# Performance work log

Hardware: AMD Instinct MI355X
Metric: run time of the kernel (lower is better)

The kernel has to match this reference:

```python
import jax, jax.numpy as jnp
import numpy as np

HIDDEN = 896
NUM_Q_HEADS = 14
NUM_KV_HEADS = 2
HEAD_DIM = 64
ROPE_BASE = 10000.0
B, S = 4, 2048


def rotate_half(x):
    x1, x2 = jnp.split(x, 2, axis=-1)
    return jnp.concatenate((-x2, x1), axis=-1)


def rope_cos_sin(position_ids):
    # position_ids: [B, S] int -> cos/sin [B, 1, S, HEAD_DIM]
    inv_freq = 1.0 / (ROPE_BASE ** (jnp.arange(0, HEAD_DIM, 2, dtype=jnp.float32) / HEAD_DIM))
    freqs = position_ids.astype(jnp.float32)[..., None] * inv_freq  # [B,S,D/2]
    emb = jnp.concatenate((freqs, freqs), axis=-1)  # [B,S,D]
    return jnp.cos(emb)[:, None, :, :], jnp.sin(emb)[:, None, :, :]


def setup_inputs() -> dict:
    key = jax.random.key(0)
    k1, k2, k3, k4, k5 = jax.random.split(key, 5)
    s = 1.0 / np.sqrt(HIDDEN)
    return {
        "hidden_states": jax.random.normal(k1, (B, S, HIDDEN), dtype=jnp.float32),
        "position_ids": jnp.broadcast_to(jnp.arange(S, dtype=jnp.int64), (B, S)),
        "Wq": jax.random.normal(k2, (HIDDEN, NUM_Q_HEADS * HEAD_DIM), dtype=jnp.float32) * s,
        "Wk": jax.random.normal(k3, (HIDDEN, NUM_KV_HEADS * HEAD_DIM), dtype=jnp.float32) * s,
        "Wv": jax.random.normal(k4, (HIDDEN, NUM_KV_HEADS * HEAD_DIM), dtype=jnp.float32) * s,
        "Wo": jax.random.normal(k5, (NUM_Q_HEADS * HEAD_DIM, HIDDEN), dtype=jnp.float32) * s,
    }


def reference(hidden_states, position_ids, Wq, Wk, Wv, Wo):
    b, s, _ = hidden_states.shape
    n_rep = NUM_Q_HEADS // NUM_KV_HEADS

    q = (hidden_states @ Wq).reshape(b, s, NUM_Q_HEADS, HEAD_DIM).transpose(0, 2, 1, 3)   # [B,Hq,S,D]
    k = (hidden_states @ Wk).reshape(b, s, NUM_KV_HEADS, HEAD_DIM).transpose(0, 2, 1, 3)  # [B,Hkv,S,D]
    v = (hidden_states @ Wv).reshape(b, s, NUM_KV_HEADS, HEAD_DIM).transpose(0, 2, 1, 3)

    cos, sin = rope_cos_sin(position_ids)  # [B,1,S,D]
    q = q * cos + rotate_half(q) * sin
    k = k * cos + rotate_half(k) * sin

    # repeat_interleave KV heads to match query heads
    k = jnp.repeat(k, n_rep, axis=1)  # [B,Hq,S,D]
    v = jnp.repeat(v, n_rep, axis=1)

    scale = 1.0 / jnp.sqrt(jnp.float32(HEAD_DIM))
    attn = jnp.einsum('bhqd,bhkd->bhqk', q, k) * scale  # [B,Hq,S,S]
    attn = jax.nn.softmax(attn, axis=-1)
    out = jnp.einsum('bhqk,bhkd->bhqd', attn, v)  # [B,Hq,S,D]
    out = out.transpose(0, 2, 1, 3).reshape(b, s, NUM_Q_HEADS * HEAD_DIM)
    return out @ Wo
```

## Files before the change

kernel.cpp:

```cpp
#include <hip/hip_runtime.h>
#include <hip/hip_bf16.h>
#include <math.h>

typedef unsigned short ushort_t;
typedef __bf16 bf16x8 __attribute__((ext_vector_type(8)));
typedef float f32x4 __attribute__((ext_vector_type(4)));

#define HIDDEN 896
#define NQH 14
#define NKVH 2
#define HD 64
#define SEQ 2048
#define NBATCH 4

__device__ inline ushort_t f2bf(float x) {
  union { float f; unsigned u; } c; c.f = x;
  unsigned r = c.u + 0x7FFFu + ((c.u >> 16) & 1u);
  return (ushort_t)(r >> 16);
}

__device__ inline unsigned pack2bf(float a, float b) {
  union { float f; unsigned u; } ca, cb; ca.f = a; cb.f = b;
  unsigned ua = ca.u + 0x8000u, ub = cb.u + 0x8000u;
  return __builtin_amdgcn_perm(ub, ua, 0x07060302);
}

__device__ inline bf16x8 ldfrag(const ushort_t* p) {
  return *reinterpret_cast<const bf16x8*>(p);
}

__device__ inline void async16(const ushort_t* g, ushort_t* l) {
  __builtin_amdgcn_global_load_lds(
      (const __attribute__((address_space(1))) void*)g,
      (__attribute__((address_space(3))) void*)l, 16, 0, 0);
}


__device__ inline void transpose_sec(const float* __restrict__ in, ushort_t* __restrict__ out,
                                     int K, int N, int bx, int by) {
  __shared__ float tile[32][33];
  int k0 = by * 32, n0 = bx * 32;
  for (int r = threadIdx.y; r < 32; r += 8) {
    int k = k0 + r, n = n0 + threadIdx.x;
    tile[r][threadIdx.x] = (k < K && n < N) ? in[(size_t)k * N + n] : 0.f;
  }
  __syncthreads();
  for (int r = threadIdx.y; r < 32; r += 8) {
    int n = n0 + r, k = k0 + threadIdx.x;
    if (n < N && k < K) out[(size_t)n * K + k] = f2bf(tile[threadIdx.x][r]);
  }
}

__global__ void k_prep(const float* __restrict__ hidden, ushort_t* __restrict__ hb,
                       const float* __restrict__ Wq, const float* __restrict__ Wk,
                       const float* __restrict__ Wv, const float* __restrict__ Wo,
                       ushort_t* __restrict__ wT, ushort_t* __restrict__ woT,
                       float2* __restrict__ ctab) {
  const int blk = blockIdx.x;
  const int tid = threadIdx.y * 32 + threadIdx.x;
  if (blk < 7168) {
    int i = blk * 256 + tid;
    float4 v = reinterpret_cast<const float4*>(hidden)[i];
    ushort4 o;
    o.x = f2bf(v.x); o.y = f2bf(v.y); o.z = f2bf(v.z); o.w = f2bf(v.w);
    reinterpret_cast<ushort4*>(hb)[i] = o;
  } else if (blk < 7424) {
    int idx = (blk - 7168) * 256 + tid;
    int s = idx >> 5, dp = idx & 31;
    float inv = exp2f(-(float)dp * 0.41524101186092596f);
    float ang = (float)s * inv;
    float sn, cn;
    sincosf(ang, &sn, &cn);
    ctab[idx] = make_float2(cn, sn);
  } else if (blk < 8208) {
    int t = blk - 7424;
    transpose_sec(Wq, wT, 896, 896, t % 28, t / 28);
  } else if (blk < 8320) {
    int t = blk - 8208;
    transpose_sec(Wk, wT + (size_t)896 * 896, 896, 128, t % 4, t / 4);
  } else if (blk < 8432) {
    int t = blk - 8320;
    transpose_sec(Wv, wT + (size_t)1024 * 896, 896, 128, t % 4, t / 4);
  } else {
    int t = blk - 8432;
    transpose_sec(Wo, woT, 896, 896, t % 28, t / 28);
  }
}

__global__ __launch_bounds__(256) void k_qkv(
    const ushort_t* __restrict__ hb,
    const ushort_t* __restrict__ wT,
    const int* __restrict__ pos_ids,
    const float2* __restrict__ ctab,
    ushort_t* __restrict__ Qg,
    ushort_t* __restrict__ Kg,
    ushort_t* __restrict__ Vtg) {
  __shared__ ushort_t smem[8192];
  ushort_t* sa = smem;
  ushort_t* sbb = smem + 4096;

  const int f = blockIdx.x;
  const int x = f & 7, s8 = f >> 3;
  const int sect = s8 % 18;
  const int mt = (s8 / 18) * 8 + x;
  const int nt0 = sect * 64;
  const int m0 = mt * 64;
  const int tid = threadIdx.x;
  const int wave = tid >> 6, lane = tid & 63;
  const int l15 = lane & 15, quad = lane >> 4;
  const int sw = l15 & 7;

  f32x4 acc[4];
  const f32x4 z4 = {0.f, 0.f, 0.f, 0.f};
#pragma unroll
  for (int b = 0; b < 4; ++b) acc[b] = z4;

  for (int kt = 0; kt < 14; ++kt) {
    const int k0 = kt * 64;
    __syncthreads();
#pragma unroll
    for (int i = 0; i < 2; ++i) {
      int id = i * 256 + tid;
      int row = id >> 3;
      int cs = (id & 7) ^ (row & 7);
      async16(hb + (size_t)(m0 + row) * HIDDEN + k0 + cs * 8, sa + (i * 256 + wave * 64) * 8);
      async16(wT + (size_t)(nt0 + row) * HIDDEN + k0 + cs * 8, sbb + (i * 256 + wave * 64) * 8);
    }
    __syncthreads();
#pragma unroll
    for (int kc = 0; kc < 2; ++kc) {
      int c = kc * 4 + quad;
      bf16x8 af = ldfrag(sa + ((wave * 16 + l15) * 8 + (c ^ sw)) * 8);
      bf16x8 bf[4];
#pragma unroll
      for (int nb = 0; nb < 4; ++nb)
        bf[nb] = ldfrag(sbb + ((nb * 16 + l15) * 8 + (c ^ sw)) * 8);
#pragma unroll
      for (int nb = 0; nb < 4; ++nb)
        acc[nb] = __builtin_amdgcn_mfma_f32_16x16x32_bf16(af, bf[nb], acc[nb], 0, 0, 0);
    }
  }

  if (sect < 16) {
    const bool isQ = sect < 14;
    const float csc = isQ ? 0.125f * 1.4426950408889634f : 1.0f;
    ushort_t* dst = isQ ? Qg : Kg;
    const int nheads = isQ ? NQH : NKVH;
    const int hh = isQ ? sect : sect - 14;
#pragma unroll
    for (int r = 0; r < 4; ++r) {
      int token = m0 + wave * 16 + quad * 4 + r;
      int b = token >> 11, s = token & 2047;
      int pos = pos_ids[token];
      size_t base = ((size_t)(b * nheads + hh) * SEQ + s) * HD;
#pragma unroll
      for (int nb = 0; nb < 2; ++nb) {
        float2 cs = ctab[pos * 32 + nb * 16 + l15];
        float x0 = acc[nb][r];
        float x1 = acc[nb + 2][r];
        float y0 = (x0 * cs.x - x1 * cs.y) * csc;
        float y1 = (x1 * cs.x + x0 * cs.y) * csc;
        dst[base + nb * 16 + l15]      = f2bf(y0);
        dst[base + nb * 16 + l15 + 32] = f2bf(y1);
      }
    }
  } else {
    const int kvh = sect - 16;
    __syncthreads();
    ushort_t* vt = smem;
    {
      int tl = wave * 16 + quad * 4;
      int chunk = tl >> 3, ofs = tl & 7;
#pragma unroll
      for (int nb = 0; nb < 4; ++nb) {
        int row = nb * 16 + l15;
        int slot = chunk ^ (row & 7);
        ushort_t* p = vt + row * 64 + slot * 8 + ofs;
        *reinterpret_cast<unsigned*>(p)     = pack2bf(acc[nb][0], acc[nb][1]);
        *reinterpret_cast<unsigned*>(p + 2) = pack2bf(acc[nb][2], acc[nb][3]);
      }
    }
    __syncthreads();
    const int bb = m0 >> 11, s0 = m0 & 2047;
#pragma unroll
    for (int i = 0; i < 2; ++i) {
      int id = i * 256 + tid;
      int row = id >> 3, ch = id & 7;
      int slot = ch ^ (row & 7);
      uint4 v = *reinterpret_cast<const uint4*>(vt + row * 64 + slot * 8);
      *reinterpret_cast<uint4*>(Vtg + ((size_t)(bb * NKVH + kvh) * HD + row) * SEQ + s0 + ch * 8) = v;
    }
  }
}

__global__ __launch_bounds__(256) void k_attn(
    const ushort_t* __restrict__ Qg,
    const ushort_t* __restrict__ Kg,
    const ushort_t* __restrict__ Vtg,
    ushort_t* __restrict__ attn) {
  __shared__ ushort_t kbuf[64 * 64];
  __shared__ ushort_t vbuf[64 * 64];
  __shared__ ushort_t pbuf[4][32 * 72];

  const int f = blockIdx.x;
  const int x = f & 7, s8 = f >> 3;
  const int lh = s8 % 7;
  const int qt = s8 / 7;
  const int b = x >> 1, kvh = x & 1;
  const int h = kvh * 7 + lh;
  const int bh = b * NQH + h;
  const int tid = threadIdx.x;
  const int wave = tid >> 6, lane = tid & 63;
  const int l15 = lane & 15, quad = lane >> 4;
  const int q0 = qt * 128;

  bf16x8 qf[2][2];
#pragma unroll
  for (int qs = 0; qs < 2; ++qs) {
    const size_t qb = ((size_t)bh * SEQ + q0 + wave * 32 + qs * 16 + l15) * HD + quad * 8;
    qf[qs][0] = ldfrag(Qg + qb);
    qf[qs][1] = ldfrag(Qg + qb + 32);
  }

  const size_t kbase = (size_t)(b * NKVH + kvh) * SEQ * HD;
  const size_t vbase = (size_t)(b * NKVH + kvh) * HD * SEQ;

  const int srow = tid >> 3;
  const int sc0 = (tid & 7) ^ (srow & 7);
  const int srow2 = (256 + tid) >> 3;
  const int sc2 = (tid & 7) ^ (srow2 & 7);
  const int sbase1 = wave * 64 * 8;
  const int sbase2 = (256 + wave * 64) * 8;

  float l_part[2] = {0.f, 0.f};
  f32x4 o[2][4];
  const f32x4 z4 = {0.f, 0.f, 0.f, 0.f};
#pragma unroll
  for (int qs = 0; qs < 2; ++qs)
#pragma unroll
    for (int nb = 0; nb < 4; ++nb) o[qs][nb] = z4;

  ushort_t* pw = pbuf[wave];

  for (int jt = 0; jt < 32; ++jt) {
    const int s0 = jt * 64;
    __syncthreads();
    async16(Kg + kbase + (size_t)(s0 + srow) * HD + sc0 * 8, kbuf + sbase1);
    async16(Vtg + vbase + (size_t)srow * SEQ + s0 + sc0 * 8, vbuf + sbase1);
    async16(Kg + kbase + (size_t)(s0 + srow2) * HD + sc2 * 8, kbuf + sbase2);
    async16(Vtg + vbase + (size_t)srow2 * SEQ + s0 + sc2 * 8, vbuf + sbase2);
    __syncthreads();

#pragma unroll
    for (int nb = 0; nb < 4; ++nb) {
      int row = nb * 16 + l15;
      int sw = row & 7;
      bf16x8 kf0 = ldfrag(kbuf + (row * 8 + (quad ^ sw)) * 8);
      bf16x8 kf1 = ldfrag(kbuf + (row * 8 + ((4 + quad) ^ sw)) * 8);
#pragma unroll
      for (int qs = 0; qs < 2; ++qs) {
        f32x4 t = z4;
        t = __builtin_amdgcn_mfma_f32_16x16x32_bf16(kf0, qf[qs][0], t, 0, 0, 0);
        t = __builtin_amdgcn_mfma_f32_16x16x32_bf16(kf1, qf[qs][1], t, 0, 0, 0);
        float p0 = __builtin_amdgcn_exp2f(t[0]);
        float p1 = __builtin_amdgcn_exp2f(t[1]);
        float p2 = __builtin_amdgcn_exp2f(t[2]);
        float p3 = __builtin_amdgcn_exp2f(t[3]);
        l_part[qs] += (p0 + p1) + (p2 + p3);
        uint2 d;
        d.x = pack2bf(p0, p1);
        d.y = pack2bf(p2, p3);
        *reinterpret_cast<uint2*>(pw + (qs * 16 + l15) * 72 + nb * 16 + quad * 4) = d;
      }
    }

    bf16x8 pf[2][2];
#pragma unroll
    for (int qs = 0; qs < 2; ++qs) {
      pf[qs][0] = ldfrag(pw + (qs * 16 + l15) * 72 + quad * 8);
      pf[qs][1] = ldfrag(pw + (qs * 16 + l15) * 72 + 32 + quad * 8);
    }
#pragma unroll
    for (int nb = 0; nb < 4; ++nb) {
      int row = nb * 16 + l15;
      int sw = row & 7;
      bf16x8 vf0 = ldfrag(vbuf + (row * 8 + (quad ^ sw)) * 8);
      bf16x8 vf1 = ldfrag(vbuf + (row * 8 + ((4 + quad) ^ sw)) * 8);
#pragma unroll
      for (int qs = 0; qs < 2; ++qs) {
        o[qs][nb] = __builtin_amdgcn_mfma_f32_16x16x32_bf16(pf[qs][0], vf0, o[qs][nb], 0, 0, 0);
        o[qs][nb] = __builtin_amdgcn_mfma_f32_16x16x32_bf16(pf[qs][1], vf1, o[qs][nb], 0, 0, 0);
      }
    }
  }

#pragma unroll
  for (int qs = 0; qs < 2; ++qs) {
    float s = l_part[qs];
    s += __shfl_xor(s, 16);
    s += __shfl_xor(s, 32);
    l_part[qs] = s;
  }

#pragma unroll
  for (int qs = 0; qs < 2; ++qs) {
    float il = 1.0f / l_part[qs];
#pragma unroll
    for (int r = 0; r < 4; ++r) {
      float inv = __shfl(il, quad * 4 + r);
      int qg = q0 + wave * 32 + qs * 16 + quad * 4 + r;
#pragma unroll
      for (int nb = 0; nb < 4; ++nb) {
        float val = o[qs][nb][r] * inv;
        attn[(size_t)(b * SEQ + qg) * (NQH * HD) + h * HD + nb * 16 + l15] = f2bf(val);
      }
    }
  }
}

__global__ __launch_bounds__(256) void k_oproj(
    const ushort_t* __restrict__ attn,
    const ushort_t* __restrict__ woT,
    float* __restrict__ out) {
  __shared__ ushort_t smem[8192];
  ushort_t* sa = smem;
  ushort_t* sbb = smem + 4096;

  const int f = blockIdx.x;
  const int x = f & 7, s8 = f >> 3;
  const int n_sect = s8 % 14;
  const int mt = (s8 / 14) * 8 + x;
  const int n0 = n_sect * 64;
  const int m0 = mt * 64;
  const int tid = threadIdx.x;
  const int wave = tid >> 6, lane = tid & 63;
  const int l15 = lane & 15, quad = lane >> 4;
  const int sw = l15 & 7;

  f32x4 acc[4];
  const f32x4 z4 = {0.f, 0.f, 0.f, 0.f};
#pragma unroll
  for (int b = 0; b < 4; ++b) acc[b] = z4;

  for (int kt = 0; kt < 14; ++kt) {
    const int k0 = kt * 64;
    __syncthreads();
#pragma unroll
    for (int i = 0; i < 2; ++i) {
      int id = i * 256 + tid;
      int row = id >> 3;
      int cs = (id & 7) ^ (row & 7);
      async16(attn + (size_t)(m0 + row) * HIDDEN + k0 + cs * 8, sa + (i * 256 + wave * 64) * 8);
      async16(woT + (size_t)(n0 + row) * HIDDEN + k0 + cs * 8, sbb + (i * 256 + wave * 64) * 8);
    }
    __syncthreads();
#pragma unroll
    for (int kc = 0; kc < 2; ++kc) {
      int c = kc * 4 + quad;
      bf16x8 af = ldfrag(sa + ((wave * 16 + l15) * 8 + (c ^ sw)) * 8);
      bf16x8 bf[4];
#pragma unroll
      for (int nb = 0; nb < 4; ++nb)
        bf[nb] = ldfrag(sbb + ((nb * 16 + l15) * 8 + (c ^ sw)) * 8);
#pragma unroll
      for (int nb = 0; nb < 4; ++nb)
        acc[nb] = __builtin_amdgcn_mfma_f32_16x16x32_bf16(af, bf[nb], acc[nb], 0, 0, 0);
    }
  }

#pragma unroll
  for (int nb = 0; nb < 4; ++nb)
#pragma unroll
    for (int r = 0; r < 4; ++r)
      out[(size_t)(m0 + wave * 16 + quad * 4 + r) * HIDDEN +
          n0 + nb * 16 + l15] = acc[nb][r];
}


extern "C" void kernel_launch(void* const* d_in, const int* in_sizes, int n_in,
                              void* d_out, int out_size, void* d_ws, size_t ws_size,
                              hipStream_t stream) {
  (void)in_sizes; (void)n_in; (void)out_size; (void)ws_size;
  const float* hidden = (const float*)d_in[0];
  const int* pos      = (const int*)d_in[1];
  const float* Wq     = (const float*)d_in[2];
  const float* Wk     = (const float*)d_in[3];
  const float* Wv     = (const float*)d_in[4];
  const float* Wo     = (const float*)d_in[5];
  float* out = (float*)d_out;

  char* ws = (char*)d_ws;
  ushort_t* hb   = (ushort_t*)(ws);
  ushort_t* wT   = (ushort_t*)(ws + 14680064);
  float2*   ctab = (float2*)  (ws + 16744448);
  ushort_t* Qg   = (ushort_t*)(ws + 17268736);
  ushort_t* Kg   = (ushort_t*)(ws + 31948800);
  ushort_t* Vtg  = (ushort_t*)(ws + 34045952);
  ushort_t* attn = (ushort_t*)(ws + 36143104);
  ushort_t* woT  = (ushort_t*)(ws + 50823168);

  k_prep<<<9216, dim3(32, 8), 0, stream>>>(hidden, hb, Wq, Wk, Wv, Wo, wT, woT, ctab);
  k_qkv<<<2304, 256, 0, stream>>>(hb, wT, pos, ctab, Qg, Kg, Vtg);
  k_attn<<<896, 256, 0, stream>>>(Qg, Kg, Vtg, attn);
  k_oproj<<<1792, 256, 0, stream>>>(attn, woT, out);
}
```

Measured before the change: 226.9 us.

## Enlarge QKV and output-projection GEMM tiles to 128x128 with 2x2 wave layout

Both projection GEMMs move from 64x64 block tiles, where each wave computed 16x64, to 128x128 tiles where each wave computes a 64x64 sub-tile of 4x4 MFMA accumulators. This raises arithmetic intensity and cuts redundant global and LDS traffic per FLOP. The QKV epilogue is reworked so each wave handles one head for RoPE, and the V transpose goes through a per-wave LDS region. In exchange, the grids shrink to 576 and 448 blocks, which may underfill the GPU's CUs, and register pressure rises.

```diff
diff --git a/kernel.cpp b/kernel.cpp
--- a/kernel.cpp
+++ b/kernel.cpp
@@ -95,100 +95,114 @@
     ushort_t* __restrict__ Qg,
     ushort_t* __restrict__ Kg,
     ushort_t* __restrict__ Vtg) {
-  __shared__ ushort_t smem[8192];
+  __shared__ ushort_t smem[16384];
   ushort_t* sa = smem;
-  ushort_t* sbb = smem + 4096;
+  ushort_t* sbb = smem + 8192;
 
   const int f = blockIdx.x;
   const int x = f & 7, s8 = f >> 3;
-  const int sect = s8 % 18;
-  const int mt = (s8 / 18) * 8 + x;
-  const int nt0 = sect * 64;
-  const int m0 = mt * 64;
+  const int nt = s8 % 9;
+  const int mt = (s8 / 9) * 8 + x;
+  const int n0 = nt * 128;
+  const int m0 = mt * 128;
   const int tid = threadIdx.x;
   const int wave = tid >> 6, lane = tid & 63;
+  const int wr = wave >> 1, wc = wave & 1;
   const int l15 = lane & 15, quad = lane >> 4;
   const int sw = l15 & 7;
 
-  f32x4 acc[4];
+  f32x4 acc[4][4];
   const f32x4 z4 = {0.f, 0.f, 0.f, 0.f};
 #pragma unroll
-  for (int b = 0; b < 4; ++b) acc[b] = z4;
+  for (int m = 0; m < 4; ++m)
+#pragma unroll
+    for (int n = 0; n < 4; ++n) acc[m][n] = z4;
 
   for (int kt = 0; kt < 14; ++kt) {
     const int k0 = kt * 64;
     __syncthreads();
 #pragma unroll
-    for (int i = 0; i < 2; ++i) {
+    for (int i = 0; i < 4; ++i) {
       int id = i * 256 + tid;
       int row = id >> 3;
       int cs = (id & 7) ^ (row & 7);
       async16(hb + (size_t)(m0 + row) * HIDDEN + k0 + cs * 8, sa + (i * 256 + wave * 64) * 8);
-      async16(wT + (size_t)(nt0 + row) * HIDDEN + k0 + cs * 8, sbb + (i * 256 + wave * 64) * 8);
+      async16(wT + (size_t)(n0 + row) * HIDDEN + k0 + cs * 8, sbb + (i * 256 + wave * 64) * 8);
     }
     __syncthreads();
 #pragma unroll
     for (int kc = 0; kc < 2; ++kc) {
       int c = kc * 4 + quad;
-      bf16x8 af = ldfrag(sa + ((wave * 16 + l15) * 8 + (c ^ sw)) * 8);
-      bf16x8 bf[4];
-#pragma unroll
-      for (int nb = 0; nb < 4; ++nb)
-        bf[nb] = ldfrag(sbb + ((nb * 16 + l15) * 8 + (c ^ sw)) * 8);
-#pragma unroll
-      for (int nb = 0; nb < 4; ++nb)
-        acc[nb] = __builtin_amdgcn_mfma_f32_16x16x32_bf16(af, bf[nb], acc[nb], 0, 0, 0);
-    }
-  }
-
-  if (sect < 16) {
-    const bool isQ = sect < 14;
+      bf16x8 af[4], bf[4];
+#pragma unroll
+      for (int m = 0; m < 4; ++m)
+        af[m] = ldfrag(sa + ((wr * 64 + m * 16 + l15) * 8 + (c ^ sw)) * 8);
+#pragma unroll
+      for (int n = 0; n < 4; ++n)
+        bf[n] = ldfrag(sbb + ((wc * 64 + n * 16 + l15) * 8 + (c ^ sw)) * 8);
+#pragma unroll
+      for (int m = 0; m < 4; ++m)
+#pragma unroll
+        for (int n = 0; n < 4; ++n)
+          acc[m][n] = __builtin_amdgcn_mfma_f32_16x16x32_bf16(af[m], bf[n], acc[m][n], 0, 0, 0);
+    }
+  }
+
+  if (nt < 8) {
+    const bool isQ = (nt < 7);
     const float csc = isQ ? 0.125f * 1.4426950408889634f : 1.0f;
     ushort_t* dst = isQ ? Qg : Kg;
     const int nheads = isQ ? NQH : NKVH;
-    const int hh = isQ ? sect : sect - 14;
-#pragma unroll
-    for (int r = 0; r < 4; ++r) {
-      int token = m0 + wave * 16 + quad * 4 + r;
-      int b = token >> 11, s = token & 2047;
-      int pos = pos_ids[token];
-      size_t base = ((size_t)(b * nheads + hh) * SEQ + s) * HD;
-#pragma unroll
-      for (int nb = 0; nb < 2; ++nb) {
-        float2 cs = ctab[pos * 32 + nb * 16 + l15];
-        float x0 = acc[nb][r];
-        float x1 = acc[nb + 2][r];
-        float y0 = (x0 * cs.x - x1 * cs.y) * csc;
-        float y1 = (x1 * cs.x + x0 * cs.y) * csc;
-        dst[base + nb * 16 + l15]      = f2bf(y0);
-        dst[base + nb * 16 + l15 + 32] = f2bf(y1);
+    const int hh = isQ ? (nt * 2 + wc) : wc;
+#pragma unroll
+    for (int m = 0; m < 4; ++m) {
+#pragma unroll
+      for (int r = 0; r < 4; ++r) {
+        int token = m0 + wr * 64 + m * 16 + quad * 4 + r;
+        int b = token >> 11, s = token & 2047;
+        int pos = pos_ids[token];
+        size_t base = ((size_t)(b * nheads + hh) * SEQ + s) * HD;
+#pragma unroll
+        for (int n = 0; n < 2; ++n) {
+          float2 cs = ctab[pos * 32 + n * 16 + l15];
+          float x0 = acc[m][n][r];
+          float x1 = acc[m][n + 2][r];
+          float y0 = (x0 * cs.x - x1 * cs.y) * csc;
+          float y1 = (x1 * cs.x + x0 * cs.y) * csc;
+          dst[base + n * 16 + l15]      = f2bf(y0);
+          dst[base + n * 16 + l15 + 32] = f2bf(y1);
+        }
       }
     }
   } else {
-    const int kvh = sect - 16;
-    __syncthreads();
-    ushort_t* vt = smem;
-    {
-      int tl = wave * 16 + quad * 4;
+    __syncthreads();
+    ushort_t* vt = smem + wave * 4096;
+#pragma unroll
+    for (int m = 0; m < 4; ++m) {
+      int tl = m * 16 + quad * 4;
       int chunk = tl >> 3, ofs = tl & 7;
 #pragma unroll
-      for (int nb = 0; nb < 4; ++nb) {
-        int row = nb * 16 + l15;
+      for (int n = 0; n < 4; ++n) {
+        int row = n * 16 + l15;
         int slot = chunk ^ (row & 7);
         ushort_t* p = vt + row * 64 + slot * 8 + ofs;
-        *reinterpret_cast<unsigned*>(p)     = pack2bf(acc[nb][0], acc[nb][1]);
-        *reinterpret_cast<unsigned*>(p + 2) = pack2bf(acc[nb][2], acc[nb][3]);
+        *reinterpret_cast<unsigned*>(p)     = pack2bf(acc[m][n][0], acc[m][n][1]);
+        *reinterpret_cast<unsigned*>(p + 2) = pack2bf(acc[m][n][2], acc[m][n][3]);
       }
     }
     __syncthreads();
-    const int bb = m0 >> 11, s0 = m0 & 2047;
-#pragma unroll
-    for (int i = 0; i < 2; ++i) {
+    const int bb = m0 >> 11, sbase = m0 & 2047;
+#pragma unroll
+    for (int i = 0; i < 8; ++i) {
       int id = i * 256 + tid;
-      int row = id >> 3, ch = id & 7;
+      int qd = id >> 9;
+      int rid = id & 511;
+      int row = rid >> 3, ch = rid & 7;
       int slot = ch ^ (row & 7);
-      uint4 v = *reinterpret_cast<const uint4*>(vt + row * 64 + slot * 8);
-      *reinterpret_cast<uint4*>(Vtg + ((size_t)(bb * NKVH + kvh) * HD + row) * SEQ + s0 + ch * 8) = v;
+      int qwr = qd >> 1, qkvh = qd & 1;
+      uint4 v = *reinterpret_cast<const uint4*>(smem + qd * 4096 + row * 64 + slot * 8);
+      *reinterpret_cast<uint4*>(
+          Vtg + ((size_t)(bb * NKVH + qkvh) * HD + row) * SEQ + sbase + qwr * 64 + ch * 8) = v;
     }
   }
 }
@@ -322,31 +336,34 @@
     const ushort_t* __restrict__ attn,
     const ushort_t* __restrict__ woT,
     float* __restrict__ out) {
-  __shared__ ushort_t smem[8192];
+  __shared__ ushort_t smem[16384];
   ushort_t* sa = smem;
-  ushort_t* sbb = smem + 4096;
+  ushort_t* sbb = smem + 8192;
 
   const int f = blockIdx.x;
   const int x = f & 7, s8 = f >> 3;
-  const int n_sect = s8 % 14;
-  const int mt = (s8 / 14) * 8 + x;
-  const int n0 = n_sect * 64;
-  const int m0 = mt * 64;
+  const int nt = s8 % 7;
+  const int mt = (s8 / 7) * 8 + x;
+  const int n0 = nt * 128;
+  const int m0 = mt * 128;
   const int tid = threadIdx.x;
   const int wave = tid >> 6, lane = tid & 63;
+  const int wr = wave >> 1, wc = wave & 1;
   const int l15 = lane & 15, quad = lane >> 4;
   const int sw = l15 & 7;
 
-  f32x4 acc[4];
+  f32x4 acc[4][4];
   const f32x4 z4 = {0.f, 0.f, 0.f, 0.f};
 #pragma unroll
-  for (int b = 0; b < 4; ++b) acc[b] = z4;
+  for (int m = 0; m < 4; ++m)
+#pragma unroll
+    for (int n = 0; n < 4; ++n) acc[m][n] = z4;
 
   for (int kt = 0; kt < 14; ++kt) {
     const int k0 = kt * 64;
     __syncthreads();
 #pragma unroll
-    for (int i = 0; i < 2; ++i) {
+    for (int i = 0; i < 4; ++i) {
       int id = i * 256 + tid;
       int row = id >> 3;
       int cs = (id & 7) ^ (row & 7);
@@ -357,23 +374,29 @@
 #pragma unroll
     for (int kc = 0; kc < 2; ++kc) {
       int c = kc * 4 + quad;
-      bf16x8 af = ldfrag(sa + ((wave * 16 + l15) * 8 + (c ^ sw)) * 8);
-      bf16x8 bf[4];
-#pragma unroll
-      for (int nb = 0; nb < 4; ++nb)
-        bf[nb] = ldfrag(sbb + ((nb * 16 + l15) * 8 + (c ^ sw)) * 8);
-#pragma unroll
-      for (int nb = 0; nb < 4; ++nb)
-        acc[nb] = __builtin_amdgcn_mfma_f32_16x16x32_bf16(af, bf[nb], acc[nb], 0, 0, 0);
-    }
-  }
-
-#pragma unroll
-  for (int nb = 0; nb < 4; ++nb)
-#pragma unroll
-    for (int r = 0; r < 4; ++r)
-      out[(size_t)(m0 + wave * 16 + quad * 4 + r) * HIDDEN +
-          n0 + nb * 16 + l15] = acc[nb][r];
+      bf16x8 af[4], bf[4];
+#pragma unroll
+      for (int m = 0; m < 4; ++m)
+        af[m] = ldfrag(sa + ((wr * 64 + m * 16 + l15) * 8 + (c ^ sw)) * 8);
+#pragma unroll
+      for (int n = 0; n < 4; ++n)
+        bf[n] = ldfrag(sbb + ((wc * 64 + n * 16 + l15) * 8 + (c ^ sw)) * 8);
+#pragma unroll
+      for (int m = 0; m < 4; ++m)
+#pragma unroll
+        for (int n = 0; n < 4; ++n)
+          acc[m][n] = __builtin_amdgcn_mfma_f32_16x16x32_bf16(af[m], bf[n], acc[m][n], 0, 0, 0);
+    }
+  }
+
+#pragma unroll
+  for (int m = 0; m < 4; ++m)
+#pragma unroll
+    for (int n = 0; n < 4; ++n)
+#pragma unroll
+      for (int r = 0; r < 4; ++r)
+        out[(size_t)(m0 + wr * 64 + m * 16 + quad * 4 + r) * HIDDEN +
+            n0 + wc * 64 + n * 16 + l15] = acc[m][n][r];
 }
 
 
@@ -400,7 +423,7 @@
   ushort_t* woT  = (ushort_t*)(ws + 50823168);
 
   k_prep<<<9216, dim3(32, 8), 0, stream>>>(hidden, hb, Wq, Wk, Wv, Wo, wT, woT, ctab);
-  k_qkv<<<2304, 256, 0, stream>>>(hb, wT, pos, ctab, Qg, Kg, Vtg);
+  k_qkv<<<576, 256, 0, stream>>>(hb, wT, pos, ctab, Qg, Kg, Vtg);
   k_attn<<<896, 256, 0, stream>>>(Qg, Kg, Vtg, attn);
-  k_oproj<<<1792, 256, 0, stream>>>(attn, woT, out);
-}
+  k_oproj<<<448, 256, 0, stream>>>(attn, woT, out);
+}
```

Measured after the change: 237.9 us. +4.8%, slower.

## Double-buffer K/V tiles in attention kernel to overlap loads with MFMA

Applied to the files above, without the earlier changes.

Splits the shared K and V tiles into two buffers and issues the async global-to-LDS loads for the next tile before computing on the current one. There is one vmcnt wait plus one barrier per tile instead of two barriers around a blocking load, so memory latency can be hidden behind QK^T, exp and PV work. It doubles LDS for K/V, which may reduce occupancy. The last iteration redundantly reloads tile 31 into the idle buffer so every iteration keeps the same shape.

```diff
diff --git a/kernel.cpp b/kernel.cpp
--- a/kernel.cpp
+++ b/kernel.cpp
@@ -198,8 +198,8 @@
     const ushort_t* __restrict__ Kg,
     const ushort_t* __restrict__ Vtg,
     ushort_t* __restrict__ attn) {
-  __shared__ ushort_t kbuf[64 * 64];
-  __shared__ ushort_t vbuf[64 * 64];
+  __shared__ ushort_t kbuf[2][64 * 64];
+  __shared__ ushort_t vbuf[2][64 * 64];
   __shared__ ushort_t pbuf[4][32 * 72];
 
   const int f = blockIdx.x;
@@ -242,21 +242,20 @@
 
   ushort_t* pw = pbuf[wave];
 
-  for (int jt = 0; jt < 32; ++jt) {
-    const int s0 = jt * 64;
-    __syncthreads();
-    async16(Kg + kbase + (size_t)(s0 + srow) * HD + sc0 * 8, kbuf + sbase1);
-    async16(Vtg + vbase + (size_t)srow * SEQ + s0 + sc0 * 8, vbuf + sbase1);
-    async16(Kg + kbase + (size_t)(s0 + srow2) * HD + sc2 * 8, kbuf + sbase2);
-    async16(Vtg + vbase + (size_t)srow2 * SEQ + s0 + sc2 * 8, vbuf + sbase2);
-    __syncthreads();
-
+  auto stage = [&](int s0, int bi) {
+    async16(Kg + kbase + (size_t)(s0 + srow) * HD + sc0 * 8, kbuf[bi] + sbase1);
+    async16(Vtg + vbase + (size_t)srow * SEQ + s0 + sc0 * 8, vbuf[bi] + sbase1);
+    async16(Kg + kbase + (size_t)(s0 + srow2) * HD + sc2 * 8, kbuf[bi] + sbase2);
+    async16(Vtg + vbase + (size_t)srow2 * SEQ + s0 + sc2 * 8, vbuf[bi] + sbase2);
+  };
+
+  auto compute = [&](const ushort_t* kb, const ushort_t* vb) {
 #pragma unroll
     for (int nb = 0; nb < 4; ++nb) {
       int row = nb * 16 + l15;
-      int sw = row & 7;
-      bf16x8 kf0 = ldfrag(kbuf + (row * 8 + (quad ^ sw)) * 8);
-      bf16x8 kf1 = ldfrag(kbuf + (row * 8 + ((4 + quad) ^ sw)) * 8);
+      int swz = row & 7;
+      bf16x8 kf0 = ldfrag(kb + (row * 8 + (quad ^ swz)) * 8);
+      bf16x8 kf1 = ldfrag(kb + (row * 8 + ((4 + quad) ^ swz)) * 8);
 #pragma unroll
       for (int qs = 0; qs < 2; ++qs) {
         f32x4 t = z4;
@@ -283,15 +282,36 @@
 #pragma unroll
     for (int nb = 0; nb < 4; ++nb) {
       int row = nb * 16 + l15;
-      int sw = row & 7;
-      bf16x8 vf0 = ldfrag(vbuf + (row * 8 + (quad ^ sw)) * 8);
-      bf16x8 vf1 = ldfrag(vbuf + (row * 8 + ((4 + quad) ^ sw)) * 8);
+      int swz = row & 7;
+      bf16x8 vf0 = ldfrag(vb + (row * 8 + (quad ^ swz)) * 8);
+      bf16x8 vf1 = ldfrag(vb + (row * 8 + ((4 + quad) ^ swz)) * 8);
 #pragma unroll
       for (int qs = 0; qs < 2; ++qs) {
         o[qs][nb] = __builtin_amdgcn_mfma_f32_16x16x32_bf16(pf[qs][0], vf0, o[qs][nb], 0, 0, 0);
         o[qs][nb] = __builtin_amdgcn_mfma_f32_16x16x32_bf16(pf[qs][1], vf1, o[qs][nb], 0, 0, 0);
       }
     }
+  };
+
+  stage(0, 0);
+  asm volatile("s_waitcnt vmcnt(0)" ::: "memory");
+  __builtin_amdgcn_s_barrier();
+  __builtin_amdgcn_sched_barrier(0);
+
+  for (int jt = 0; jt < 32; jt += 2) {
+    stage((jt + 1) * 64, 1);
+    compute(kbuf[0], vbuf[0]);
+    __builtin_amdgcn_sched_barrier(0);
+    asm volatile("s_waitcnt vmcnt(0)" ::: "memory");
+    __builtin_amdgcn_s_barrier();
+    __builtin_amdgcn_sched_barrier(0);
+
+    stage(jt + 2 < 32 ? (jt + 2) * 64 : (jt + 1) * 64, 0);
+    compute(kbuf[1], vbuf[1]);
+    __builtin_amdgcn_sched_barrier(0);
+    asm volatile("s_waitcnt vmcnt(0)" ::: "memory");
+    __builtin_amdgcn_s_barrier();
+    __builtin_amdgcn_sched_barrier(0);
   }
 
 #pragma unroll
```

Measured after the change: 243.4 us. +7.3%, slower.
